# Kernel optimization log

Measured on AMD Instinct MI355X. Metric: run time of the kernel, lower is better.

The kernel has to match this reference:

```python
import jax, jax.numpy as jnp
import numpy as np

B, S, C, M, L = 32, 8192, 64, 16, 4  # batch, seq, n_enc, n_modes, n_layers


def setup_inputs() -> dict:
    key = jax.random.key(0)
    ks = jax.random.split(key, 12)
    scale = 1.0 / (C * M)
    return {
        "input_tensor": jax.random.normal(ks[0], (B, S, 1), dtype=jnp.float32),
        "enc_w": jax.random.normal(ks[1], (C, 1), dtype=jnp.float32) * 0.1,
        "enc_b": jax.random.normal(ks[2], (C,), dtype=jnp.float32) * 0.1,
        "R_re": jax.random.normal(ks[3], (L, C, C, M), dtype=jnp.float32) * scale,
        "R_im": jax.random.normal(ks[4], (L, C, C, M), dtype=jnp.float32) * scale,
        "Wl_w": jax.random.normal(ks[5], (L, C, C), dtype=jnp.float32) * 0.1,
        "Wl_b": jax.random.normal(ks[6], (L, C), dtype=jnp.float32) * 0.1,
        "d1_w": jax.random.normal(ks[7], (C, C), dtype=jnp.float32) * 0.1,
        "d1_b": jax.random.normal(ks[8], (C,), dtype=jnp.float32) * 0.1,
        "d2_w": jax.random.normal(ks[9], (1, C), dtype=jnp.float32) * 0.1,
        "d2_b": jax.random.normal(ks[10], (1,), dtype=jnp.float32) * 0.1,
    }


def reference(input_tensor, enc_w, enc_b, R_re, R_im, Wl_w, Wl_b, d1_w, d1_b, d2_w, d2_b):
    # encoder: Conv1d(1, C, k=1) == per-position dense over channel dim
    h = jnp.einsum('bsi,ci->bsc', input_tensor, enc_w) + enc_b  # [B,S,C]
    n_freq = S // 2 + 1
    for l in range(L):
        x_cs = jnp.swapaxes(h, 1, 2)                 # [B,C,S]
        x_ft = jnp.fft.rfft(x_cs, axis=-1)           # [B,C,n_freq] complex
        Rl = R_re[l] + 1j * R_im[l]                  # [C,C,M]
        y = jnp.einsum('bim,iom->bom', x_ft[:, :, :M], Rl)  # [B,C,M]
        y_full = jnp.concatenate(
            [y, jnp.zeros((B, C, n_freq - M), dtype=y.dtype)], axis=-1)
        spat = jnp.fft.irfft(y_full, n=S, axis=-1)   # [B,C,S] float32
        wout = jnp.einsum('oi,bis->bos', Wl_w[l], x_cs) + Wl_b[l][None, :, None]
        h = jax.nn.gelu(jnp.swapaxes(spat + wout, 1, 2), approximate=False)
    z = jax.nn.gelu(jnp.einsum('bsc,oc->bso', h, d1_w) + d1_b, approximate=False)
    out = jnp.einsum('bso,po->bsp', z, d2_w) + d2_b  # [B,S,1]
    return out
```

## Files before the change

kernel.cpp:

```cpp
#include <hip/hip_runtime.h>
#include <math.h>

#define NB 32
#define NS 8192
#define NC 64
#define NM 16
#define NL 4
#define NM2 32
#define NSBF 32
#define TPOS 64
#define PAD 65

typedef float f16v __attribute__((ext_vector_type(16)));

static __device__ __forceinline__ f16v zero16() {
    f16v v;
    #pragma unroll
    for (int j = 0; j < 16; ++j) v[j] = 0.0f;
    return v;
}

static __device__ __forceinline__ float gelu_exact(float v) {
    return 0.5f * v * (1.0f + erff(v * 0.7071067811865475f));
}

__global__ void k_table(float* __restrict__ T) {
    int s = blockIdx.x * blockDim.x + threadIdx.x;
    if (s >= NS) return;
    const float w = 6.283185307179586f / (float)NS;
    float* row = T + (size_t)s * NM2;
    #pragma unroll
    for (int m = 0; m < NM; ++m) {
        int idx = (m * s) & (NS - 1);
        float a = w * (float)idx;
        float sv, cv;
        sincosf(a, &sv, &cv);
        row[2*m]   = cv;
        row[2*m+1] = sv;
    }
}

__global__ void k_prep(const float* __restrict__ Ww, const float* __restrict__ d1w,
                       float* __restrict__ Wt, float* __restrict__ d1t) {
    int idx = blockIdx.x * 256 + threadIdx.x;
    if (idx < NL*NC*NC) {
        int l = idx / (NC*NC), r = idx % (NC*NC);
        int i = r / NC, o = r % NC;
        Wt[idx] = Ww[(size_t)l*NC*NC + (size_t)o*NC + i];
    } else if (idx < NL*NC*NC + NC*NC) {
        int r = idx - NL*NC*NC;
        int i = r / NC, o = r % NC;
        d1t[r] = d1w[(size_t)o*NC + i];
    }
}

__global__ void __launch_bounds__(256) k_enc(const float* __restrict__ x,
                                             const float* __restrict__ ew,
                                             const float* __restrict__ eb,
                                             float* __restrict__ h) {
    int p = blockIdx.x * blockDim.x + threadIdx.x;
    float xv = x[p];
    float4* out = (float4*)(h + (size_t)p * NC);
    #pragma unroll
    for (int q = 0; q < NC/4; ++q) {
        float4 w4 = ((const float4*)ew)[q];
        float4 b4 = ((const float4*)eb)[q];
        out[q] = make_float4(fmaf(xv, w4.x, b4.x), fmaf(xv, w4.y, b4.y),
                             fmaf(xv, w4.z, b4.z), fmaf(xv, w4.w, b4.w));
    }
}

__global__ void __launch_bounds__(256) k_fwd(const float* __restrict__ h,
                                             const float* __restrict__ T,
                                             float* __restrict__ partial) {
    __shared__ float red[4 * NC * 33];
    int b = blockIdx.y, sb = blockIdx.x;
    int t = threadIdx.x;
    int w = t >> 6, lane = t & 63;
    const int PPW = NS / NSBF / 4;
    f16v A0 = zero16(), A1 = zero16();
    int s0 = sb * (NS / NSBF) + w * PPW;
    const float* hp = h + ((size_t)b*NS + s0)*NC + lane;
    #pragma unroll 2
    for (int it = 0; it < PPW; ++it) {
        float hv = hp[(size_t)it * NC];
        int su = __builtin_amdgcn_readfirstlane(s0 + it);
        const f16v* tr = (const f16v*)(T + (size_t)su * NM2);
        A0 += hv * tr[0];
        A1 += hv * tr[1];
    }
    float* rr = &red[(w*NC + lane) * 33];
    #pragma unroll
    for (int j = 0; j < 16; ++j) rr[j] = A0[j];
    #pragma unroll
    for (int j = 0; j < 16; ++j) rr[16 + j] = A1[j];
    __syncthreads();
    float* pout = partial + ((size_t)b*NSBF + sb) * (NC*NM2);
    #pragma unroll
    for (int e = 0; e < (NC*NM2)/256; ++e) {
        int idx = t + 256*e;
        int c = idx >> 5, k = idx & 31;
        pout[idx] = red[c*33 + k] + red[(NC + c)*33 + k]
                  + red[(2*NC + c)*33 + k] + red[(3*NC + c)*33 + k];
    }
}

__global__ void __launch_bounds__(256) k_mix(const float* __restrict__ partial,
                                             const float* __restrict__ Rre,
                                             const float* __restrict__ Rim,
                                             float* __restrict__ yst, int l) {
    __shared__ float xf[NC*NM2];
    int b = blockIdx.x, jg = blockIdx.y, t = threadIdx.x;
    #pragma unroll
    for (int e = 0; e < (NC*NM2)/256; ++e) {
        int idx = t + 256*e;
        float s = 0.f;
        #pragma unroll 8
        for (int sb = 0; sb < NSBF; ++sb)
            s += partial[((size_t)b*NSBF + sb)*(NC*NM2) + idx];
        xf[idx] = s;
    }
    __syncthreads();
    {
        int p = t + 256*jg;
        int o = p >> 4, m = p & 15;
        float yre = 0.f, yim = 0.f;
        #pragma unroll 8
        for (int i = 0; i < NC; ++i) {
            float xr = xf[i*NM2 + 2*m];
            float xs = xf[i*NM2 + 2*m + 1];
            size_t ridx = (((size_t)l*NC + i)*NC + o)*NM + m;
            float rr = Rre[ridx], ri = Rim[ridx];
            yre = fmaf(xr, rr, yre); yre = fmaf(xs, ri, yre);
            yim = fmaf(xr, ri, yim); yim = fmaf(-xs, rr, yim);
        }
        float* yb = yst + (size_t)b*NM2*NC;
        if (m == 0) { yb[o] = yre * (1.0f/NS); yb[NC + o] = 0.f; }
        else {
            yb[(size_t)(2*m)*NC + o]   = yre * (2.0f/NS);
            yb[(size_t)(2*m+1)*NC + o] = -yim * (2.0f/NS);
        }
    }
}

__global__ void __launch_bounds__(256) k_spec(float* __restrict__ h,
                                              const float* __restrict__ yst,
                                              const float* __restrict__ Wt,
                                              const float* __restrict__ Wb,
                                              int l) {
    __shared__ float hs[TPOS * PAD];
    int b = blockIdx.y;
    int t = threadIdx.x;
    int og = __builtin_amdgcn_readfirstlane(t >> 6);
    int p  = t & 63;
    int s0 = blockIdx.x * TPOS;
    int s  = s0 + p;

    const float4* hblk = (const float4*)(h + ((size_t)b*NS + s0)*NC);
    float4 l0 = hblk[t];
    float4 l1 = hblk[t + 256];
    float4 l2 = hblk[t + 512];
    float4 l3 = hblk[t + 768];
    {
        int ss = t >> 4, q = t & 15;
        float* d = &hs[ss*PAD + 4*q];
        d[0] = l0.x; d[1] = l0.y; d[2] = l0.z; d[3] = l0.w;
        d = &hs[(ss+16)*PAD + 4*q];
        d[0] = l1.x; d[1] = l1.y; d[2] = l1.z; d[3] = l1.w;
        d = &hs[(ss+32)*PAD + 4*q];
        d[0] = l2.x; d[1] = l2.y; d[2] = l2.z; d[3] = l2.w;
        d = &hs[(ss+48)*PAD + 4*q];
        d[0] = l3.x; d[1] = l3.y; d[2] = l3.z; d[3] = l3.w;
    }
    __syncthreads();

    const float* Wl = Wt + (size_t)l*NC*NC + og*16;
    const float* bl = Wb + (size_t)l*NC + og*16;
    const float* yb = yst + (size_t)b*NM2*NC + og*16;

    f16v acc = *(const f16v*)bl;

    {
        acc += *(const f16v*)yb;
        float ang = (float)s * (6.283185307179586f / (float)NS);
        float c1, s1;
        sincosf(ang, &s1, &c1);
        float cm = c1, sm = s1;
        #pragma unroll 1
        for (int m = 1; m < NM; ++m) {
            f16v yc = *(const f16v*)(yb + (size_t)(2*m)*NC);
            f16v ysv = *(const f16v*)(yb + (size_t)(2*m+1)*NC);
            acc += cm * yc;
            acc += sm * ysv;
            float cn = cm*c1 - sm*s1;
            sm = cm*s1 + sm*c1;
            cm = cn;
        }
    }

    const float* hrow = &hs[p * PAD];
    #pragma unroll 4
    for (int i = 0; i < NC; ++i) {
        float hv = hrow[i];
        f16v w = *(const f16v*)(Wl + (size_t)i*NC);
        acc += hv * w;
    }

    float* hp = h + ((size_t)b*NS + s)*NC + og*16;
    f16v g;
    #pragma unroll
    for (int j = 0; j < 16; ++j) g[j] = gelu_exact(acc[j]);
    *(f16v*)hp = g;
}

__global__ void __launch_bounds__(256) k_dec(const float* __restrict__ h,
                                             const float* __restrict__ d1t,
                                             const float* __restrict__ d1b,
                                             const float* __restrict__ d2w,
                                             const float* __restrict__ d2b,
                                             float* __restrict__ out) {
    __shared__ float hs[TPOS * PAD];
    __shared__ float red[4 * TPOS];
    int t = threadIdx.x;
    int og = __builtin_amdgcn_readfirstlane(t >> 6);
    int p  = t & 63;
    int p0 = blockIdx.x * TPOS;

    const float4* hblk = (const float4*)(h + (size_t)p0 * NC);
    float4 l0 = hblk[t];
    float4 l1 = hblk[t + 256];
    float4 l2 = hblk[t + 512];
    float4 l3 = hblk[t + 768];
    {
        int ss = t >> 4, q = t & 15;
        float* d = &hs[ss*PAD + 4*q];
        d[0] = l0.x; d[1] = l0.y; d[2] = l0.z; d[3] = l0.w;
        d = &hs[(ss+16)*PAD + 4*q];
        d[0] = l1.x; d[1] = l1.y; d[2] = l1.z; d[3] = l1.w;
        d = &hs[(ss+32)*PAD + 4*q];
        d[0] = l2.x; d[1] = l2.y; d[2] = l2.z; d[3] = l2.w;
        d = &hs[(ss+48)*PAD + 4*q];
        d[0] = l3.x; d[1] = l3.y; d[2] = l3.z; d[3] = l3.w;
    }
    __syncthreads();

    f16v acc = *(const f16v*)(d1b + og*16);
    const float* hrow = &hs[p * PAD];
    #pragma unroll 4
    for (int i = 0; i < NC; ++i) {
        float hv = hrow[i];
        f16v w = *(const f16v*)(d1t + (size_t)i*NC + og*16);
        acc += hv * w;
    }
    float res = 0.f;
    #pragma unroll
    for (int j = 0; j < 16; ++j)
        res = fmaf(gelu_exact(acc[j]), d2w[og*16 + j], res);
    red[og*TPOS + p] = res;
    __syncthreads();
    if (t < TPOS) {
        out[p0 + t] = d2b[0] + red[t] + red[TPOS + t]
                    + red[2*TPOS + t] + red[3*TPOS + t];
    }
}

extern "C" void kernel_launch(void* const* d_in, const int* in_sizes, int n_in,
                              void* d_out, int out_size, void* d_ws, size_t ws_size,
                              hipStream_t stream) {
    const float* input = (const float*)d_in[0];
    const float* enc_w = (const float*)d_in[1];
    const float* enc_b = (const float*)d_in[2];
    const float* R_re  = (const float*)d_in[3];
    const float* R_im  = (const float*)d_in[4];
    const float* Wl_w  = (const float*)d_in[5];
    const float* Wl_b  = (const float*)d_in[6];
    const float* d1_w  = (const float*)d_in[7];
    const float* d1_b  = (const float*)d_in[8];
    const float* d2_w  = (const float*)d_in[9];
    const float* d2_b  = (const float*)d_in[10];
    float* out = (float*)d_out;

    float* ws  = (float*)d_ws;
    float* h   = ws;
    float* T   = h   + (size_t)NB*NS*NC;
    float* par = T   + (size_t)NS*NM2;
    float* yst = par + (size_t)NB*NSBF*NC*NM2;
    float* Wt  = yst + (size_t)NB*NM2*NC;
    float* d1t = Wt  + (size_t)NL*NC*NC;

    hipLaunchKernelGGL(k_table, dim3(NS/256), dim3(256), 0, stream, T);
    hipLaunchKernelGGL(k_prep, dim3((NL*NC*NC + NC*NC + 255)/256), dim3(256), 0,
                       stream, Wl_w, d1_w, Wt, d1t);
    hipLaunchKernelGGL(k_enc, dim3((NB*NS)/256), dim3(256), 0, stream,
                       input, enc_w, enc_b, h);
    for (int l = 0; l < NL; ++l) {
        hipLaunchKernelGGL(k_fwd, dim3(NSBF, NB), dim3(256), 0, stream, h, T, par);
        hipLaunchKernelGGL(k_mix, dim3(NB, 4), dim3(256), 0, stream,
                           par, R_re, R_im, yst, l);
        hipLaunchKernelGGL(k_spec, dim3(NS/TPOS, NB), dim3(256), 0, stream,
                           h, yst, Wt, Wl_b, l);
    }
    hipLaunchKernelGGL(k_dec, dim3((NB*NS)/TPOS), dim3(256), 0, stream,
                       h, d1t, d1_b, d2_w, d2_b, out);
}
```

Before: 432.2 us.

## Process two positions per thread in spectral and decoder kernels; coalesce encoder stores

```diff
diff --git a/kernel.cpp b/kernel.cpp
--- a/kernel.cpp
+++ b/kernel.cpp
@@ -8,7 +8,7 @@
 #define NL 4
 #define NM2 32
 #define NSBF 32
-#define TPOS 64
+#define TPOS 128
 #define PAD 65
 
 typedef float f16v __attribute__((ext_vector_type(16)));
@@ -58,15 +58,18 @@
                                              const float* __restrict__ ew,
                                              const float* __restrict__ eb,
                                              float* __restrict__ h) {
-    int p = blockIdx.x * blockDim.x + threadIdx.x;
-    float xv = x[p];
-    float4* out = (float4*)(h + (size_t)p * NC);
-    #pragma unroll
-    for (int q = 0; q < NC/4; ++q) {
+    int t = threadIdx.x;
+    int base = blockIdx.x * 64;
+    float4* hout = (float4*)(h + (size_t)base * NC);
+    #pragma unroll
+    for (int j = 0; j < 4; ++j) {
+        int idx = t + 256*j;
+        int sl = idx >> 4, q = idx & 15;
+        float xv = x[base + sl];
         float4 w4 = ((const float4*)ew)[q];
         float4 b4 = ((const float4*)eb)[q];
-        out[q] = make_float4(fmaf(xv, w4.x, b4.x), fmaf(xv, w4.y, b4.y),
-                             fmaf(xv, w4.z, b4.z), fmaf(xv, w4.w, b4.w));
+        hout[idx] = make_float4(fmaf(xv, w4.x, b4.x), fmaf(xv, w4.y, b4.y),
+                                fmaf(xv, w4.z, b4.z), fmaf(xv, w4.w, b4.w));
     }
 }
 
@@ -154,63 +157,81 @@
     int og = __builtin_amdgcn_readfirstlane(t >> 6);
     int p  = t & 63;
     int s0 = blockIdx.x * TPOS;
-    int s  = s0 + p;
 
     const float4* hblk = (const float4*)(h + ((size_t)b*NS + s0)*NC);
-    float4 l0 = hblk[t];
-    float4 l1 = hblk[t + 256];
-    float4 l2 = hblk[t + 512];
-    float4 l3 = hblk[t + 768];
-    {
-        int ss = t >> 4, q = t & 15;
-        float* d = &hs[ss*PAD + 4*q];
-        d[0] = l0.x; d[1] = l0.y; d[2] = l0.z; d[3] = l0.w;
-        d = &hs[(ss+16)*PAD + 4*q];
-        d[0] = l1.x; d[1] = l1.y; d[2] = l1.z; d[3] = l1.w;
-        d = &hs[(ss+32)*PAD + 4*q];
-        d[0] = l2.x; d[1] = l2.y; d[2] = l2.z; d[3] = l2.w;
-        d = &hs[(ss+48)*PAD + 4*q];
-        d[0] = l3.x; d[1] = l3.y; d[2] = l3.z; d[3] = l3.w;
-    }
-    __syncthreads();
+    float4 ld0 = hblk[t];
+    float4 ld1 = hblk[t + 256];
+    float4 ld2 = hblk[t + 512];
+    float4 ld3 = hblk[t + 768];
+    float4 ld4 = hblk[t + 1024];
+    float4 ld5 = hblk[t + 1280];
+    float4 ld6 = hblk[t + 1536];
+    float4 ld7 = hblk[t + 1792];
 
     const float* Wl = Wt + (size_t)l*NC*NC + og*16;
     const float* bl = Wb + (size_t)l*NC + og*16;
     const float* yb = yst + (size_t)b*NM2*NC + og*16;
 
-    f16v acc = *(const f16v*)bl;
+    f16v accA = *(const f16v*)bl;
+    f16v accB = accA;
 
     {
-        acc += *(const f16v*)yb;
-        float ang = (float)s * (6.283185307179586f / (float)NS);
-        float c1, s1;
-        sincosf(ang, &s1, &c1);
-        float cm = c1, sm = s1;
+        f16v y0 = *(const f16v*)yb;
+        accA += y0;
+        accB += y0;
+        const float w1 = 6.283185307179586f / (float)NS;
+        float angA = (float)(s0 + p) * w1;
+        float angB = (float)(s0 + p + 64) * w1;
+        float cA1, sA1, cB1, sB1;
+        sincosf(angA, &sA1, &cA1);
+        sincosf(angB, &sB1, &cB1);
+        float cmA = cA1, smA = sA1, cmB = cB1, smB = sB1;
         #pragma unroll 1
         for (int m = 1; m < NM; ++m) {
-            f16v yc = *(const f16v*)(yb + (size_t)(2*m)*NC);
+            f16v yc  = *(const f16v*)(yb + (size_t)(2*m)*NC);
             f16v ysv = *(const f16v*)(yb + (size_t)(2*m+1)*NC);
-            acc += cm * yc;
-            acc += sm * ysv;
-            float cn = cm*c1 - sm*s1;
-            sm = cm*s1 + sm*c1;
-            cm = cn;
+            accA += cmA * yc;  accA += smA * ysv;
+            accB += cmB * yc;  accB += smB * ysv;
+            float cnA = cmA*cA1 - smA*sA1;
+            smA = cmA*sA1 + smA*cA1;  cmA = cnA;
+            float cnB = cmB*cB1 - smB*sB1;
+            smB = cmB*sB1 + smB*cB1;  cmB = cnB;
         }
     }
 
-    const float* hrow = &hs[p * PAD];
-    #pragma unroll 4
+    {
+        int ss = t >> 4, q4 = (t & 15) * 4;
+        float* d;
+        d = &hs[ss*PAD + q4];        d[0]=ld0.x; d[1]=ld0.y; d[2]=ld0.z; d[3]=ld0.w;
+        d = &hs[(ss+16)*PAD + q4];   d[0]=ld1.x; d[1]=ld1.y; d[2]=ld1.z; d[3]=ld1.w;
+        d = &hs[(ss+32)*PAD + q4];   d[0]=ld2.x; d[1]=ld2.y; d[2]=ld2.z; d[3]=ld2.w;
+        d = &hs[(ss+48)*PAD + q4];   d[0]=ld3.x; d[1]=ld3.y; d[2]=ld3.z; d[3]=ld3.w;
+        d = &hs[(ss+64)*PAD + q4];   d[0]=ld4.x; d[1]=ld4.y; d[2]=ld4.z; d[3]=ld4.w;
+        d = &hs[(ss+80)*PAD + q4];   d[0]=ld5.x; d[1]=ld5.y; d[2]=ld5.z; d[3]=ld5.w;
+        d = &hs[(ss+96)*PAD + q4];   d[0]=ld6.x; d[1]=ld6.y; d[2]=ld6.z; d[3]=ld6.w;
+        d = &hs[(ss+112)*PAD + q4];  d[0]=ld7.x; d[1]=ld7.y; d[2]=ld7.z; d[3]=ld7.w;
+    }
+    __syncthreads();
+
+    const float* hA = &hs[p * PAD];
+    const float* hB = &hs[(p + 64) * PAD];
+    #pragma unroll 8
     for (int i = 0; i < NC; ++i) {
-        float hv = hrow[i];
+        float va = hA[i], vb = hB[i];
         f16v w = *(const f16v*)(Wl + (size_t)i*NC);
-        acc += hv * w;
-    }
-
-    float* hp = h + ((size_t)b*NS + s)*NC + og*16;
+        accA += va * w;
+        accB += vb * w;
+    }
+
+    float* hpA = h + ((size_t)b*NS + s0 + p)*NC + og*16;
+    float* hpB = h + ((size_t)b*NS + s0 + p + 64)*NC + og*16;
     f16v g;
     #pragma unroll
-    for (int j = 0; j < 16; ++j) g[j] = gelu_exact(acc[j]);
-    *(f16v*)hp = g;
+    for (int j = 0; j < 16; ++j) g[j] = gelu_exact(accA[j]);
+    *(f16v*)hpA = g;
+    #pragma unroll
+    for (int j = 0; j < 16; ++j) g[j] = gelu_exact(accB[j]);
+    *(f16v*)hpB = g;
 }
 
 __global__ void __launch_bounds__(256) k_dec(const float* __restrict__ h,
@@ -227,36 +248,48 @@
     int p0 = blockIdx.x * TPOS;
 
     const float4* hblk = (const float4*)(h + (size_t)p0 * NC);
-    float4 l0 = hblk[t];
-    float4 l1 = hblk[t + 256];
-    float4 l2 = hblk[t + 512];
-    float4 l3 = hblk[t + 768];
+    float4 ld0 = hblk[t];
+    float4 ld1 = hblk[t + 256];
+    float4 ld2 = hblk[t + 512];
+    float4 ld3 = hblk[t + 768];
+    float4 ld4 = hblk[t + 1024];
+    float4 ld5 = hblk[t + 1280];
+    float4 ld6 = hblk[t + 1536];
+    float4 ld7 = hblk[t + 1792];
     {
-        int ss = t >> 4, q = t & 15;
-        float* d = &hs[ss*PAD + 4*q];
-        d[0] = l0.x; d[1] = l0.y; d[2] = l0.z; d[3] = l0.w;
-        d = &hs[(ss+16)*PAD + 4*q];
-        d[0] = l1.x; d[1] = l1.y; d[2] = l1.z; d[3] = l1.w;
-        d = &hs[(ss+32)*PAD + 4*q];
-        d[0] = l2.x; d[1] = l2.y; d[2] = l2.z; d[3] = l2.w;
-        d = &hs[(ss+48)*PAD + 4*q];
-        d[0] = l3.x; d[1] = l3.y; d[2] = l3.z; d[3] = l3.w;
-    }
-    __syncthreads();
-
-    f16v acc = *(const f16v*)(d1b + og*16);
-    const float* hrow = &hs[p * PAD];
-    #pragma unroll 4
+        int ss = t >> 4, q4 = (t & 15) * 4;
+        float* d;
+        d = &hs[ss*PAD + q4];        d[0]=ld0.x; d[1]=ld0.y; d[2]=ld0.z; d[3]=ld0.w;
+        d = &hs[(ss+16)*PAD + q4];   d[0]=ld1.x; d[1]=ld1.y; d[2]=ld1.z; d[3]=ld1.w;
+        d = &hs[(ss+32)*PAD + q4];   d[0]=ld2.x; d[1]=ld2.y; d[2]=ld2.z; d[3]=ld2.w;
+        d = &hs[(ss+48)*PAD + q4];   d[0]=ld3.x; d[1]=ld3.y; d[2]=ld3.z; d[3]=ld3.w;
+        d = &hs[(ss+64)*PAD + q4];   d[0]=ld4.x; d[1]=ld4.y; d[2]=ld4.z; d[3]=ld4.w;
+        d = &hs[(ss+80)*PAD + q4];   d[0]=ld5.x; d[1]=ld5.y; d[2]=ld5.z; d[3]=ld5.w;
+        d = &hs[(ss+96)*PAD + q4];   d[0]=ld6.x; d[1]=ld6.y; d[2]=ld6.z; d[3]=ld6.w;
+        d = &hs[(ss+112)*PAD + q4];  d[0]=ld7.x; d[1]=ld7.y; d[2]=ld7.z; d[3]=ld7.w;
+    }
+    __syncthreads();
+
+    f16v accA = *(const f16v*)(d1b + og*16);
+    f16v accB = accA;
+    const float* hA = &hs[p * PAD];
+    const float* hB = &hs[(p + 64) * PAD];
+    #pragma unroll 8
     for (int i = 0; i < NC; ++i) {
-        float hv = hrow[i];
+        float va = hA[i], vb = hB[i];
         f16v w = *(const f16v*)(d1t + (size_t)i*NC + og*16);
-        acc += hv * w;
-    }
-    float res = 0.f;
-    #pragma unroll
-    for (int j = 0; j < 16; ++j)
-        res = fmaf(gelu_exact(acc[j]), d2w[og*16 + j], res);
-    red[og*TPOS + p] = res;
+        accA += va * w;
+        accB += vb * w;
+    }
+    float resA = 0.f, resB = 0.f;
+    #pragma unroll
+    for (int j = 0; j < 16; ++j) {
+        float dw = d2w[og*16 + j];
+        resA = fmaf(gelu_exact(accA[j]), dw, resA);
+        resB = fmaf(gelu_exact(accB[j]), dw, resB);
+    }
+    red[og*TPOS + p]      = resA;
+    red[og*TPOS + p + 64] = resB;
     __syncthreads();
     if (t < TPOS) {
         out[p0 + t] = d2b[0] + red[t] + red[TPOS + t]
@@ -291,7 +324,7 @@
     hipLaunchKernelGGL(k_table, dim3(NS/256), dim3(256), 0, stream, T);
     hipLaunchKernelGGL(k_prep, dim3((NL*NC*NC + NC*NC + 255)/256), dim3(256), 0,
                        stream, Wl_w, d1_w, Wt, d1t);
-    hipLaunchKernelGGL(k_enc, dim3((NB*NS)/256), dim3(256), 0, stream,
+    hipLaunchKernelGGL(k_enc, dim3((NB*NS)/64), dim3(256), 0, stream,
                        input, enc_w, enc_b, h);
     for (int l = 0; l < NL; ++l) {
         hipLaunchKernelGGL(k_fwd, dim3(NSBF, NB), dim3(256), 0, stream, h, T, par);
```

New measurement: 402.7 us. 1.07x faster.
